# Kernel optimization log

Hardware: AMD Instinct MI355X
Metric: run time of the kernel (lower is better)

The kernel has to match this reference:

```python
import jax, jax.numpy as jnp
import numpy as np

N = 1_000_000
HID = 128
S = 10_000

def setup_inputs() -> dict:
    key = jax.random.key(0)
    k1, k2, k3, k4, k5 = jax.random.split(key, 5)
    seg_embs = jax.random.normal(k1, (N, HID), dtype=jnp.float32)
    owners = jnp.sort(jax.random.randint(k2, (N,), 0, S, dtype=jnp.int64))
    W_proj = jax.random.normal(k3, (HID, HID), dtype=jnp.float32) * (1.0 / np.sqrt(HID))
    b_proj = jax.random.normal(k4, (HID,), dtype=jnp.float32) * 0.02
    w_score = jax.random.normal(k5, (HID,), dtype=jnp.float32) * (1.0 / np.sqrt(HID))
    b_score = jnp.zeros((), dtype=jnp.float32)
    return {"seg_embs": seg_embs, "owners": owners, "W_proj": W_proj,
            "b_proj": b_proj, "w_score": w_score, "b_score": b_score,
            "num_segments": S}

def reference(seg_embs, owners, W_proj, b_proj, w_score, b_score, num_segments):
    # H = tanh(Linear(seg_embs)); u = score(H)  -> [N]
    H = jnp.tanh(seg_embs @ W_proj.T + b_proj)            # [N, hid]
    u = H @ w_score + b_score                              # [N]
    # per-owner (segment) stable softmax
    umax = jax.ops.segment_max(u, owners, num_segments=num_segments)   # [S]
    e = jnp.exp(u - umax[owners])                          # [N]
    denom = jax.ops.segment_sum(e, owners, num_segments=num_segments)  # [S]
    a = e / denom[owners]                                  # [N]
    # weighted sum of seg_embs per owner -> [S, hid]
    z = jax.ops.segment_sum(a[:, None] * seg_embs, owners, num_segments=num_segments)
    return z
```

## Files before the change

kernel.cpp:

```cpp
#include <hip/hip_runtime.h>
#include <hip/hip_bf16.h>
#include <cmath>

#define HID 128
#define TM 64
#define MAXK 8
#define PIECE_F 132
#define XP 132

typedef __attribute__((ext_vector_type(8))) short bf16x8;
typedef __attribute__((ext_vector_type(16))) float f32x16;
typedef __attribute__((ext_vector_type(4))) float f32x4;
typedef __attribute__((ext_vector_type(2))) float f32x2;

__device__ __forceinline__ float exp2_fast(float x) {
    float r;
    asm("v_exp_f32 %0, %1" : "=v"(r) : "v"(x));
    return r;
}

__device__ __forceinline__ float fast_tanh(float x) {
    float e = exp2_fast(x * 2.885390082f);
    return 1.0f - 2.0f * __builtin_amdgcn_rcpf(e + 1.0f);
}

__device__ __forceinline__ bf16x8 pack8(const float* f) {
    union { short h8[8]; bf16x8 v; } u;
    #pragma unroll
    for (int q = 0; q < 8; ++q)
        u.h8[q] = (short)__bfloat16_as_ushort(__float2bfloat16(f[q]));
    return u.v;
}

__global__ __launch_bounds__(256) void prep_kernel(
    const int* __restrict__ ow, int* __restrict__ seg_start,
    int* __restrict__ fseg, const float* __restrict__ W,
    short* __restrict__ whi, int N, int S)
{
    const int b = blockIdx.x;
    if (b < 8) {
        int id = b * 256 + threadIdx.x;
        int l  = id & 63;
        int kc = (id >> 6) & 7;
        int wv = id >> 9;
        int j  = wv * 32 + (l & 31);
        int k0 = kc * 16 + ((l >> 5) << 3);
        const float* src = W + j * HID + k0;
        float a8[8];
        #pragma unroll
        for (int q = 0; q < 8; ++q) a8[q] = src[q];
        *(bf16x8*)(whi + (size_t)id * 8) = pack8(a8);
        return;
    }
    const int is64 = (ow[(size_t)N - 1] == 0) ? 1 : 0;
    long i = (long)(b - 8) * 256 + threadIdx.x;
    if (i > N) return;
    int a = (i == 0) ? -1 : ow[is64 ? (size_t)(2 * (i - 1)) : (size_t)(i - 1)];
    int bb = (i == N) ? S : ow[is64 ? (size_t)(2 * i) : (size_t)i];
    for (int s = a + 1; s <= bb; ++s) seg_start[s] = (int)i;
    if (i < N && (i & (TM - 1)) == 0) fseg[i >> 6] = bb;
}

__global__ __launch_bounds__(256, 4) void fused_kernel(
    const float* __restrict__ X, const short* __restrict__ whi_g,
    const float* __restrict__ bproj, const float* __restrict__ wscore,
    const int* __restrict__ seg_start, const int* __restrict__ fseg,
    float* __restrict__ pieces, int N, int S)
{
    __shared__ __align__(16) short X_lds[TM * XP];
    __shared__ float u_part[4][TM];
    __shared__ float w_lds[TM];
    __shared__ float bw_lds[2 * HID];

    const int tid  = threadIdx.x;
    const int bIdx = blockIdx.x;
    const int rbase = bIdx * TM;
    const int limit = (N - rbase < TM) ? (N - rbase) : TM;

    const int lane = tid & 63;
    const int wv   = tid >> 6;
    const int l31  = lane & 31;
    const int hig  = lane >> 5;

    bf16x8 wf[8];
    #pragma unroll
    for (int kc = 0; kc < 8; ++kc)
        wf[kc] = *(const bf16x8*)(whi_g + (size_t)((wv * 8 + kc) * 64 + lane) * 8);

    const int sseg0 = fseg[bIdx];
    int svl = sseg0 + lane;
    int sv  = seg_start[(svl <= S) ? svl : S];

    #pragma unroll
    for (int it = 0; it < 4; ++it) {
        int id = it * 256 + tid;
        int r  = id >> 4;
        int c  = id & 15;
        int grow = rbase + r;
        if (grow >= N) grow = N - 1;
        float a8[8];
        *(f32x4*)(a8)     = *(const f32x4*)(X + (size_t)grow * HID + c * 8);
        *(f32x4*)(a8 + 4) = *(const f32x4*)(X + (size_t)grow * HID + c * 8 + 4);
        *(bf16x8*)(&X_lds[r * XP + c * 8]) = pack8(a8);
    }
    if (tid < HID) {
        bw_lds[2 * tid]     = bproj[tid];
        bw_lds[2 * tid + 1] = wscore[tid];
    }
    __syncthreads();

    f32x16 acc0, acc1;
    #pragma unroll
    for (int g = 0; g < 16; ++g) { acc0[g] = 0.0f; acc1[g] = 0.0f; }

    #pragma unroll
    for (int kc = 0; kc < 8; ++kc) {
        int c = kc * 2 + hig;
        bf16x8 x0 = *(const bf16x8*)(&X_lds[l31 * XP + c * 8]);
        bf16x8 x1 = *(const bf16x8*)(&X_lds[(32 + l31) * XP + c * 8]);
        acc0 = __builtin_amdgcn_mfma_f32_32x32x16_bf16(wf[kc], x0, acc0, 0, 0, 0);
        acc1 = __builtin_amdgcn_mfma_f32_32x32x16_bf16(wf[kc], x1, acc1, 0, 0, 0);
    }

    float s0 = 0.0f, s1 = 0.0f;
    #pragma unroll
    for (int reg = 0; reg < 16; ++reg) {
        int j = wv * 32 + (reg & 3) + ((reg >> 2) << 3) + (hig << 2);
        f32x2 bw = *(const f32x2*)(&bw_lds[2 * j]);
        s0 = fmaf(fast_tanh(acc0[reg] + bw.x), bw.y, s0);
        s1 = fmaf(fast_tanh(acc1[reg] + bw.x), bw.y, s1);
    }
    s0 += __shfl_xor(s0, 32, 64);
    s1 += __shfl_xor(s1, 32, 64);
    if (hig == 0) {
        u_part[wv][l31]      = s0;
        u_part[wv][32 + l31] = s1;
    }
    __syncthreads();

    for (int i = wv; ; i += 4) {
        int st, en;
        if (i < 63) {
            st = __shfl(sv, i, 64);
            en = __shfl(sv, i + 1, 64);
        } else {
            int s0i = sseg0 + i;
            st = seg_start[(s0i     <= S) ? s0i     : S];
            en = seg_start[(s0i + 1 <= S) ? s0i + 1 : S];
        }
        if (st >= rbase + limit) break;
        if (en <= st) continue;
        int a  = st - rbase; if (a < 0) a = 0;
        int bb = en - rbase; if (bb > limit) bb = limit;
        if (a >= bb) continue;

        float uv = -INFINITY;
        if (a + lane < bb)
            uv = u_part[0][a + lane] + u_part[1][a + lane]
               + u_part[2][a + lane] + u_part[3][a + lane];
        float m = uv;
        #pragma unroll
        for (int o = 32; o > 0; o >>= 1) m = fmaxf(m, __shfl_xor(m, o, 64));
        float e0 = (a + lane < bb) ? exp2_fast((uv - m) * 1.442695041f) : 0.0f;
        float d = e0;
        #pragma unroll
        for (int o = 32; o > 0; o >>= 1) d += __shfl_xor(d, o, 64);
        if (a + lane < bb) w_lds[a + lane] = e0;

        f32x2 p = {0.0f, 0.0f};
        int rr = a;
        for (; rr + 4 <= bb; rr += 4) {
            #pragma unroll
            for (int q = 0; q < 4; ++q) {
                int rc = rr + q;
                float wq = w_lds[rc];
                unsigned pr = *(const unsigned*)(&X_lds[rc * XP + 2 * lane]);
                float x0 = __builtin_bit_cast(float, pr << 16);
                float x1 = __builtin_bit_cast(float, pr & 0xFFFF0000u);
                p.x = fmaf(wq, x0, p.x);
                p.y = fmaf(wq, x1, p.y);
            }
        }
        for (; rr < bb; ++rr) {
            float wq = w_lds[rr];
            unsigned pr = *(const unsigned*)(&X_lds[rr * XP + 2 * lane]);
            float x0 = __builtin_bit_cast(float, pr << 16);
            float x1 = __builtin_bit_cast(float, pr & 0xFFFF0000u);
            p.x = fmaf(wq, x0, p.x);
            p.y = fmaf(wq, x1, p.y);
        }

        int sseg = sseg0 + i;
        int slot = (bIdx - (st >> 6)) & (MAXK - 1);
        float* dst = pieces + ((size_t)sseg * MAXK + slot) * PIECE_F;
        if (lane == 0) { dst[0] = m; dst[1] = d; }
        *(f32x2*)(dst + 4 + 2 * lane) = p;
    }
}

__global__ __launch_bounds__(256) void fixup_kernel(
    const float* __restrict__ pieces, const int* __restrict__ seg_start,
    float* __restrict__ z, int S)
{
    const int s = blockIdx.x * 4 + (threadIdx.x >> 6);
    if (s >= S) return;
    const int lane = threadIdx.x & 63;
    const int start = seg_start[s];
    const int end   = seg_start[s + 1];

    if (start >= end) {
        f32x2 zo = {0.0f, 0.0f};
        *(f32x2*)(z + (size_t)s * HID + lane * 2) = zo;
        return;
    }
    int K = ((end - 1) >> 6) - (start >> 6) + 1;
    if (K > MAXK) K = MAXK;

    const float* base0 = pieces + (size_t)s * MAXK * PIECE_F;
    float M = -INFINITY;
    for (int k = 0; k < K; ++k) M = fmaxf(M, base0[k * PIECE_F]);

    float D = 0.0f;
    f32x2 zz = {0.0f, 0.0f};
    for (int k = 0; k < K; ++k) {
        const float* b = base0 + k * PIECE_F;
        float sc = __expf(b[0] - M);
        D = fmaf(b[1], sc, D);
        f32x2 pv = *(const f32x2*)(b + 4 + lane * 2);
        zz.x = fmaf(sc, pv.x, zz.x);
        zz.y = fmaf(sc, pv.y, zz.y);
    }
    float inv = 1.0f / D;
    f32x2 zo = {zz.x * inv, zz.y * inv};
    *(f32x2*)(z + (size_t)s * HID + lane * 2) = zo;
}

extern "C" void kernel_launch(void* const* d_in, const int* in_sizes, int n_in,
                              void* d_out, int out_size, void* d_ws, size_t ws_size,
                              hipStream_t stream)
{
    const float* X   = (const float*)d_in[0];
    const int*   ow  = (const int*)  d_in[1];
    const float* W   = (const float*)d_in[2];
    const float* bp  = (const float*)d_in[3];
    const float* wsc = (const float*)d_in[4];

    const int N  = in_sizes[0] / HID;
    const int S  = out_size / HID;
    const int NT = (N + TM - 1) / TM;

    char* ws = (char*)d_ws;
    size_t off_seg = 0;
    size_t off_fs  = (((size_t)(S + 1) * 4) + 255) & ~(size_t)255;
    size_t off_w   = (off_fs + (size_t)NT * 4 + 255) & ~(size_t)255;
    size_t off_pc  = (off_w + (size_t)HID * HID * 2 + 255) & ~(size_t)255;

    int*   seg    = (int*)  (ws + off_seg);
    int*   fsg    = (int*)  (ws + off_fs);
    short* whi    = (short*)(ws + off_w);
    float* pieces = (float*)(ws + off_pc);
    float* z      = (float*)d_out;

    const int blocksSeg = ((N + 1) + 255) / 256;
    prep_kernel<<<blocksSeg + 8, 256, 0, stream>>>(ow, seg, fsg, W, whi, N, S);

    fused_kernel<<<NT, 256, 0, stream>>>(X, whi, bp, wsc, seg, fsg,
                                         pieces, N, S);

    fixup_kernel<<<(S + 3) / 4, 256, 0, stream>>>(pieces, seg, z, S);
}
```

Before: 124.1 us.

## Make fused kernel persistent with register prefetch of next X tile

The fused kernel now runs on a fixed grid of at most 768 blocks that loop over row tiles. Each block loads the next tile's X rows into registers while it computes the current one. This is meant to hide global-load latency and to save the per-block cost of reloading W fragments. In exchange it uses 32 more VGPRs for the prefetch buffer, lowers launch bounds occupancy from 4 to 3 blocks per CU, and adds an extra barrier per tile.

```diff
diff --git a/kernel.cpp b/kernel.cpp
--- a/kernel.cpp
+++ b/kernel.cpp
@@ -7,6 +7,7 @@
 #define MAXK 8
 #define PIECE_F 132
 #define XP 132
+#define GRID_F 768
 
 typedef __attribute__((ext_vector_type(8))) short bf16x8;
 typedef __attribute__((ext_vector_type(16))) float f32x16;
@@ -61,11 +62,11 @@
     if (i < N && (i & (TM - 1)) == 0) fseg[i >> 6] = bb;
 }
 
-__global__ __launch_bounds__(256, 4) void fused_kernel(
+__global__ __launch_bounds__(256, 3) void fused_kernel(
     const float* __restrict__ X, const short* __restrict__ whi_g,
     const float* __restrict__ bproj, const float* __restrict__ wscore,
     const int* __restrict__ seg_start, const int* __restrict__ fseg,
-    float* __restrict__ pieces, int N, int S)
+    float* __restrict__ pieces, int N, int S, int NT)
 {
     __shared__ __align__(16) short X_lds[TM * XP];
     __shared__ float u_part[4][TM];
@@ -73,10 +74,6 @@
     __shared__ float bw_lds[2 * HID];
 
     const int tid  = threadIdx.x;
-    const int bIdx = blockIdx.x;
-    const int rbase = bIdx * TM;
-    const int limit = (N - rbase < TM) ? (N - rbase) : TM;
-
     const int lane = tid & 63;
     const int wv   = tid >> 6;
     const int l31  = lane & 31;
@@ -87,114 +84,154 @@
     for (int kc = 0; kc < 8; ++kc)
         wf[kc] = *(const bf16x8*)(whi_g + (size_t)((wv * 8 + kc) * 64 + lane) * 8);
 
-    const int sseg0 = fseg[bIdx];
-    int svl = sseg0 + lane;
-    int sv  = seg_start[(svl <= S) ? svl : S];
-
-    #pragma unroll
-    for (int it = 0; it < 4; ++it) {
-        int id = it * 256 + tid;
-        int r  = id >> 4;
-        int c  = id & 15;
-        int grow = rbase + r;
-        if (grow >= N) grow = N - 1;
-        float a8[8];
-        *(f32x4*)(a8)     = *(const f32x4*)(X + (size_t)grow * HID + c * 8);
-        *(f32x4*)(a8 + 4) = *(const f32x4*)(X + (size_t)grow * HID + c * 8 + 4);
-        *(bf16x8*)(&X_lds[r * XP + c * 8]) = pack8(a8);
-    }
     if (tid < HID) {
         bw_lds[2 * tid]     = bproj[tid];
         bw_lds[2 * tid + 1] = wscore[tid];
     }
-    __syncthreads();
-
-    f32x16 acc0, acc1;
-    #pragma unroll
-    for (int g = 0; g < 16; ++g) { acc0[g] = 0.0f; acc1[g] = 0.0f; }
-
-    #pragma unroll
-    for (int kc = 0; kc < 8; ++kc) {
-        int c = kc * 2 + hig;
-        bf16x8 x0 = *(const bf16x8*)(&X_lds[l31 * XP + c * 8]);
-        bf16x8 x1 = *(const bf16x8*)(&X_lds[(32 + l31) * XP + c * 8]);
-        acc0 = __builtin_amdgcn_mfma_f32_32x32x16_bf16(wf[kc], x0, acc0, 0, 0, 0);
-        acc1 = __builtin_amdgcn_mfma_f32_32x32x16_bf16(wf[kc], x1, acc1, 0, 0, 0);
-    }
-
-    float s0 = 0.0f, s1 = 0.0f;
-    #pragma unroll
-    for (int reg = 0; reg < 16; ++reg) {
-        int j = wv * 32 + (reg & 3) + ((reg >> 2) << 3) + (hig << 2);
-        f32x2 bw = *(const f32x2*)(&bw_lds[2 * j]);
-        s0 = fmaf(fast_tanh(acc0[reg] + bw.x), bw.y, s0);
-        s1 = fmaf(fast_tanh(acc1[reg] + bw.x), bw.y, s1);
-    }
-    s0 += __shfl_xor(s0, 32, 64);
-    s1 += __shfl_xor(s1, 32, 64);
-    if (hig == 0) {
-        u_part[wv][l31]      = s0;
-        u_part[wv][32 + l31] = s1;
-    }
-    __syncthreads();
-
-    for (int i = wv; ; i += 4) {
-        int st, en;
-        if (i < 63) {
-            st = __shfl(sv, i, 64);
-            en = __shfl(sv, i + 1, 64);
-        } else {
-            int s0i = sseg0 + i;
-            st = seg_start[(s0i     <= S) ? s0i     : S];
-            en = seg_start[(s0i + 1 <= S) ? s0i + 1 : S];
-        }
-        if (st >= rbase + limit) break;
-        if (en <= st) continue;
-        int a  = st - rbase; if (a < 0) a = 0;
-        int bb = en - rbase; if (bb > limit) bb = limit;
-        if (a >= bb) continue;
-
-        float uv = -INFINITY;
-        if (a + lane < bb)
-            uv = u_part[0][a + lane] + u_part[1][a + lane]
-               + u_part[2][a + lane] + u_part[3][a + lane];
-        float m = uv;
-        #pragma unroll
-        for (int o = 32; o > 0; o >>= 1) m = fmaxf(m, __shfl_xor(m, o, 64));
-        float e0 = (a + lane < bb) ? exp2_fast((uv - m) * 1.442695041f) : 0.0f;
-        float d = e0;
-        #pragma unroll
-        for (int o = 32; o > 0; o >>= 1) d += __shfl_xor(d, o, 64);
-        if (a + lane < bb) w_lds[a + lane] = e0;
-
-        f32x2 p = {0.0f, 0.0f};
-        int rr = a;
-        for (; rr + 4 <= bb; rr += 4) {
+
+    const int nB = gridDim.x;
+    f32x4 pf[8];
+
+    {
+        long rb = (long)blockIdx.x * TM;
+        #pragma unroll
+        for (int i = 0; i < 8; ++i) {
+            int id = (i >> 1) * 256 + tid;
+            int r  = id >> 4;
+            int c  = id & 15;
+            long grow = rb + r;
+            if (grow >= N) grow = N - 1;
+            pf[i] = *(const f32x4*)(X + (size_t)grow * HID + c * 8 + (i & 1) * 4);
+        }
+    }
+
+    for (int T = blockIdx.x; T < NT; T += nB) {
+        const int rbase = T * TM;
+        const int limit = (N - rbase < TM) ? (N - rbase) : TM;
+
+        const int sseg0 = fseg[T];
+        int svl = sseg0 + lane;
+        int sv  = seg_start[(svl <= S) ? svl : S];
+
+        #pragma unroll
+        for (int it = 0; it < 4; ++it) {
+            int id = it * 256 + tid;
+            int r  = id >> 4;
+            int c  = id & 15;
+            float a8[8];
+            *(f32x4*)(a8)     = pf[2 * it];
+            *(f32x4*)(a8 + 4) = pf[2 * it + 1];
+            *(bf16x8*)(&X_lds[r * XP + c * 8]) = pack8(a8);
+        }
+        asm volatile("s_waitcnt lgkmcnt(0)" ::: "memory");
+        __builtin_amdgcn_s_barrier();
+
+        {
+            int Tn = T + nB;
+            if (Tn < NT) {
+                long rb = (long)Tn * TM;
+                #pragma unroll
+                for (int i = 0; i < 8; ++i) {
+                    int id = (i >> 1) * 256 + tid;
+                    int r  = id >> 4;
+                    int c  = id & 15;
+                    long grow = rb + r;
+                    if (grow >= N) grow = N - 1;
+                    pf[i] = *(const f32x4*)(X + (size_t)grow * HID + c * 8 + (i & 1) * 4);
+                }
+            }
+        }
+
+        f32x16 acc0, acc1;
+        #pragma unroll
+        for (int g = 0; g < 16; ++g) { acc0[g] = 0.0f; acc1[g] = 0.0f; }
+
+        #pragma unroll
+        for (int kc = 0; kc < 8; ++kc) {
+            int c = kc * 2 + hig;
+            bf16x8 x0 = *(const bf16x8*)(&X_lds[l31 * XP + c * 8]);
+            bf16x8 x1 = *(const bf16x8*)(&X_lds[(32 + l31) * XP + c * 8]);
+            acc0 = __builtin_amdgcn_mfma_f32_32x32x16_bf16(wf[kc], x0, acc0, 0, 0, 0);
+            acc1 = __builtin_amdgcn_mfma_f32_32x32x16_bf16(wf[kc], x1, acc1, 0, 0, 0);
+        }
+
+        float s0 = 0.0f, s1 = 0.0f;
+        #pragma unroll
+        for (int reg = 0; reg < 16; ++reg) {
+            int j = wv * 32 + (reg & 3) + ((reg >> 2) << 3) + (hig << 2);
+            f32x2 bw = *(const f32x2*)(&bw_lds[2 * j]);
+            s0 = fmaf(fast_tanh(acc0[reg] + bw.x), bw.y, s0);
+            s1 = fmaf(fast_tanh(acc1[reg] + bw.x), bw.y, s1);
+        }
+        s0 += __shfl_xor(s0, 32, 64);
+        s1 += __shfl_xor(s1, 32, 64);
+        if (hig == 0) {
+            u_part[wv][l31]      = s0;
+            u_part[wv][32 + l31] = s1;
+        }
+        asm volatile("s_waitcnt lgkmcnt(0)" ::: "memory");
+        __builtin_amdgcn_s_barrier();
+
+        for (int i = wv; ; i += 4) {
+            int st, en;
+            if (i < 63) {
+                st = __shfl(sv, i, 64);
+                en = __shfl(sv, i + 1, 64);
+            } else {
+                int s0i = sseg0 + i;
+                st = seg_start[(s0i     <= S) ? s0i     : S];
+                en = seg_start[(s0i + 1 <= S) ? s0i + 1 : S];
+            }
+            if (st >= rbase + limit) break;
+            if (en <= st) continue;
+            int a  = st - rbase; if (a < 0) a = 0;
+            int bb = en - rbase; if (bb > limit) bb = limit;
+            if (a >= bb) continue;
+
+            float uv = -INFINITY;
+            if (a + lane < bb)
+                uv = u_part[0][a + lane] + u_part[1][a + lane]
+                   + u_part[2][a + lane] + u_part[3][a + lane];
+            float m = uv;
             #pragma unroll
-            for (int q = 0; q < 4; ++q) {
-                int rc = rr + q;
-                float wq = w_lds[rc];
-                unsigned pr = *(const unsigned*)(&X_lds[rc * XP + 2 * lane]);
+            for (int o = 32; o > 0; o >>= 1) m = fmaxf(m, __shfl_xor(m, o, 64));
+            float e0 = (a + lane < bb) ? exp2_fast((uv - m) * 1.442695041f) : 0.0f;
+            float d = e0;
+            #pragma unroll
+            for (int o = 32; o > 0; o >>= 1) d += __shfl_xor(d, o, 64);
+            if (a + lane < bb) w_lds[a + lane] = e0;
+
+            f32x2 p = {0.0f, 0.0f};
+            int rr = a;
+            for (; rr + 4 <= bb; rr += 4) {
+                #pragma unroll
+                for (int q = 0; q < 4; ++q) {
+                    int rc = rr + q;
+                    float wq = w_lds[rc];
+                    unsigned pr = *(const unsigned*)(&X_lds[rc * XP + 2 * lane]);
+                    float x0 = __builtin_bit_cast(float, pr << 16);
+                    float x1 = __builtin_bit_cast(float, pr & 0xFFFF0000u);
+                    p.x = fmaf(wq, x0, p.x);
+                    p.y = fmaf(wq, x1, p.y);
+                }
+            }
+            for (; rr < bb; ++rr) {
+                float wq = w_lds[rr];
+                unsigned pr = *(const unsigned*)(&X_lds[rr * XP + 2 * lane]);
                 float x0 = __builtin_bit_cast(float, pr << 16);
                 float x1 = __builtin_bit_cast(float, pr & 0xFFFF0000u);
                 p.x = fmaf(wq, x0, p.x);
                 p.y = fmaf(wq, x1, p.y);
             }
-        }
-        for (; rr < bb; ++rr) {
-            float wq = w_lds[rr];
-            unsigned pr = *(const unsigned*)(&X_lds[rr * XP + 2 * lane]);
-            float x0 = __builtin_bit_cast(float, pr << 16);
-            float x1 = __builtin_bit_cast(float, pr & 0xFFFF0000u);
-            p.x = fmaf(wq, x0, p.x);
-            p.y = fmaf(wq, x1, p.y);
-        }
-
-        int sseg = sseg0 + i;
-        int slot = (bIdx - (st >> 6)) & (MAXK - 1);
-        float* dst = pieces + ((size_t)sseg * MAXK + slot) * PIECE_F;
-        if (lane == 0) { dst[0] = m; dst[1] = d; }
-        *(f32x2*)(dst + 4 + 2 * lane) = p;
+
+            int sseg = sseg0 + i;
+            int slot = (T - (st >> 6)) & (MAXK - 1);
+            float* dst = pieces + ((size_t)sseg * MAXK + slot) * PIECE_F;
+            if (lane == 0) { dst[0] = m; dst[1] = d; }
+            *(f32x2*)(dst + 4 + 2 * lane) = p;
+        }
+        asm volatile("s_waitcnt lgkmcnt(0)" ::: "memory");
+        __builtin_amdgcn_s_barrier();
     }
 }
 
@@ -264,8 +301,9 @@
     const int blocksSeg = ((N + 1) + 255) / 256;
     prep_kernel<<<blocksSeg + 8, 256, 0, stream>>>(ow, seg, fsg, W, whi, N, S);
 
-    fused_kernel<<<NT, 256, 0, stream>>>(X, whi, bp, wsc, seg, fsg,
-                                         pieces, N, S);
+    const int grid = (NT < GRID_F) ? NT : GRID_F;
+    fused_kernel<<<grid, 256, 0, stream>>>(X, whi, bp, wsc, seg, fsg,
+                                           pieces, N, S, NT);
 
     fixup_kernel<<<(S + 3) / 4, 256, 0, stream>>>(pieces, seg, z, S);
 }
```

Result: slower. 136.2 us (+9.8%).
